# Kernel tuning notes

Measured on AMD Instinct MI355X. Metric: run time of the kernel, lower is better.

Reference implementation:

```python
import jax, jax.numpy as jnp
import numpy as np

B, N, M = 8, 4096, 4096


def setup_inputs() -> dict:
    key = jax.random.key(0)
    ks = jax.random.split(key, 8)
    return {
        "x_aligned": jax.random.normal(ks[0], (B, N, 3), dtype=jnp.float32),
        "y": jax.random.normal(ks[1], (B, M, 3), dtype=jnp.float32),
        "R": jax.random.normal(ks[2], (B, 3, 3), dtype=jnp.float32),
        "S": jax.random.normal(ks[3], (B, 3), dtype=jnp.float32),
        "t": jax.random.normal(ks[4], (B, 3, 1), dtype=jnp.float32),
        "R_gt": jax.random.normal(ks[5], (B, 3, 3), dtype=jnp.float32),
        "S_gt": jax.random.normal(ks[6], (B, 3), dtype=jnp.float32),
        "t_gt": jax.random.normal(ks[7], (B, 3), dtype=jnp.float32),
    }


def chamfer_distance(x, y):
    # x: [B,N,3], y: [B,M,3]; bidirectional mean squared NN distance
    xn = jnp.sum(x * x, axis=-1)                      # [B,N]
    yn = jnp.sum(y * y, axis=-1)                      # [B,M]
    xy = jnp.einsum('bnd,bmd->bnm', x, y)             # [B,N,M]
    d2 = xn[:, :, None] + yn[:, None, :] - 2.0 * xy   # [B,N,M] squared dists
    cham_x = jnp.mean(jnp.min(d2, axis=2), axis=1)    # [B] x -> y
    cham_y = jnp.mean(jnp.min(d2, axis=1), axis=1)    # [B] y -> x
    return jnp.mean(cham_x) + jnp.mean(cham_y)        # batch mean, summed dirs


def reference(x_aligned, y, R, S, t, R_gt, S_gt, t_gt):
    t = jnp.squeeze(t)                                # [B,3]
    eye = jnp.eye(3, dtype=R.dtype)
    R_loss = jnp.einsum('bij,bkj->bik', R, R_gt) - eye  # R @ R_gt^T - I
    L_reg = (jnp.sum(R_loss * R_loss)
             + jnp.sum((S - S_gt) ** 2)
             + jnp.sum((t - t_gt) ** 2))
    L_chamfer = chamfer_distance(x_aligned, y)
    return L_reg + L_chamfer
```

## Files before the change

### kernel.cpp

```cpp
#include <hip/hip_runtime.h>

#define BB 8
#define NN 4096
#define MC 256
#define NCHUNK (NN / MC)
#define KPT 8
#define TPB 256
#define PTS_PER_BLOCK (TPB * KPT)
#define NPTS (2 * BB * NN)


__global__ __launch_bounds__(TPB) void chamfer_partial(
    const float* __restrict__ X, const float* __restrict__ Y,
    float* __restrict__ partial) {
  __shared__ float4 ly[MC];
  const int tid = threadIdx.x;
  const int zb  = blockIdx.z;
  const int b   = zb & (BB - 1);
  const int dir = zb >> 3;
  const float* pts  = dir ? (Y + b * NN * 3) : (X + b * NN * 3);
  const float* refs = dir ? (X + b * NN * 3) : (Y + b * NN * 3);
  const int c = blockIdx.y;

  {
    const int j = c * MC + tid;
    const float a0 = refs[j * 3 + 0];
    const float a1 = refs[j * 3 + 1];
    const float a2 = refs[j * 3 + 2];
    ly[tid] = make_float4(-2.0f * a0, -2.0f * a1, -2.0f * a2,
                          a0 * a0 + a1 * a1 + a2 * a2);
  }
  __syncthreads();

  float px[KPT], py[KPT], pz[KPT], m[KPT];
  const int p0 = blockIdx.x * PTS_PER_BLOCK + tid;
#pragma unroll
  for (int k = 0; k < KPT; k++) {
    const int p = p0 + k * TPB;
    px[k] = pts[p * 3 + 0];
    py[k] = pts[p * 3 + 1];
    pz[k] = pts[p * 3 + 2];
    m[k] = 1e30f;
  }

#pragma unroll 2
  for (int j = 0; j < MC; j += 2) {
    const float4 w0 = ly[j];
    const float4 w1 = ly[j + 1];
#pragma unroll
    for (int k = 0; k < KPT; k++) {
      const float s0 = fmaf(px[k], w0.x, fmaf(py[k], w0.y, fmaf(pz[k], w0.z, w0.w)));
      const float s1 = fmaf(px[k], w1.x, fmaf(py[k], w1.y, fmaf(pz[k], w1.z, w1.w)));
      m[k] = fminf(m[k], fminf(s0, s1));
    }
  }

#pragma unroll
  for (int k = 0; k < KPT; k++) {
    const int p = p0 + k * TPB;
    const float pn = px[k] * px[k] + py[k] * py[k] + pz[k] * pz[k];
    partial[(c * (2 * BB) + zb) * NN + p] = m[k] + pn;
  }
}

__global__ __launch_bounds__(256) void chamfer_reduce(
    const float* __restrict__ partial,
    const float* __restrict__ R, const float* __restrict__ S,
    const float* __restrict__ t, const float* __restrict__ Rgt,
    const float* __restrict__ Sgt, const float* __restrict__ tgt,
    float* __restrict__ out) {
  const int tid = threadIdx.x;
  const int q0 = blockIdx.x * 1024 + tid;
  float s = 0.0f;
#pragma unroll
  for (int kk = 0; kk < 4; kk++) {
    const int q = q0 + kk * 256;
    float m = 1e30f;
#pragma unroll
    for (int c = 0; c < NCHUNK; c++)
      m = fminf(m, partial[c * NPTS + q]);
    s += m;
  }
  for (int o = 32; o > 0; o >>= 1) s += __shfl_down(s, o);
  __shared__ float wsum[4];
  if ((tid & 63) == 0) wsum[tid >> 6] = s;
  __syncthreads();
  if (tid == 0) {
    const float bs = wsum[0] + wsum[1] + wsum[2] + wsum[3];
    atomicAdd(out, bs * (1.0f / (float)(BB * NN)));
  }

  if (blockIdx.x == 0) {
    float v = 0.0f;
    if (tid < 72) {
      const int b = tid / 9, ik = tid % 9, i = ik / 3, k = ik % 3;
      const float* Rb = R + b * 9;
      const float* Gb = Rgt + b * 9;
      float d = Rb[i * 3 + 0] * Gb[k * 3 + 0] +
                Rb[i * 3 + 1] * Gb[k * 3 + 1] +
                Rb[i * 3 + 2] * Gb[k * 3 + 2];
      d -= (i == k) ? 1.0f : 0.0f;
      v = d * d;
    } else if (tid < 96) {
      const int i = tid - 72;
      const float d = S[i] - Sgt[i];
      v = d * d;
    } else if (tid < 120) {
      const int i = tid - 96;
      const float d = t[i] - tgt[i];
      v = d * d;
    }
    for (int o = 32; o > 0; o >>= 1) v += __shfl_down(v, o);
    __shared__ float rsum[4];
    if ((tid & 63) == 0) rsum[tid >> 6] = v;
    __syncthreads();
    if (tid == 0) atomicAdd(out, rsum[0] + rsum[1] + rsum[2] + rsum[3]);
  }
}

extern "C" void kernel_launch(void* const* d_in, const int* in_sizes, int n_in,
                              void* d_out, int out_size, void* d_ws, size_t ws_size,
                              hipStream_t stream) {
  const float* X   = (const float*)d_in[0];
  const float* Y   = (const float*)d_in[1];
  const float* R   = (const float*)d_in[2];
  const float* S   = (const float*)d_in[3];
  const float* t   = (const float*)d_in[4];
  const float* Rgt = (const float*)d_in[5];
  const float* Sgt = (const float*)d_in[6];
  const float* tgt = (const float*)d_in[7];

  float* partial = (float*)d_ws;
  float* out     = (float*)d_out;

  hipMemsetAsync(out, 0, sizeof(float), stream);

  dim3 gA(NN / PTS_PER_BLOCK, NCHUNK, 2 * BB);
  chamfer_partial<<<gA, TPB, 0, stream>>>(X, Y, partial);

  chamfer_reduce<<<NPTS / 1024, 256, 0, stream>>>(partial, R, S, t, Rgt, Sgt, tgt, out);
}
```

Before: 94.56 us.

## Halve points per thread, prefetch LDS refs, fold memset into kernel

Reduces points per thread from 8 to 4, doubling the block count of the distance kernel for better occupancy across CUs. The inner loop now processes four reference points per step and prefetches the next four from LDS. The separate memset of the output is replaced by zeroing it inside the first kernel, and the reduce kernel uses more blocks with one point per thread. The trade-off is lower register reuse per LDS read and more atomics in the reduction.

Measured after the change: 91.46 us. 1.03x faster.

```diff
diff --git a/kernel.cpp b/kernel.cpp
--- a/kernel.cpp
+++ b/kernel.cpp
@@ -4,7 +4,7 @@
 #define NN 4096
 #define MC 256
 #define NCHUNK (NN / MC)
-#define KPT 8
+#define KPT 4
 #define TPB 256
 #define PTS_PER_BLOCK (TPB * KPT)
 #define NPTS (2 * BB * NN)
@@ -12,7 +12,7 @@
 
 __global__ __launch_bounds__(TPB) void chamfer_partial(
     const float* __restrict__ X, const float* __restrict__ Y,
-    float* __restrict__ partial) {
+    float* __restrict__ partial, float* __restrict__ out) {
   __shared__ float4 ly[MC];
   const int tid = threadIdx.x;
   const int zb  = blockIdx.z;
@@ -21,6 +21,9 @@
   const float* pts  = dir ? (Y + b * NN * 3) : (X + b * NN * 3);
   const float* refs = dir ? (X + b * NN * 3) : (Y + b * NN * 3);
   const int c = blockIdx.y;
+
+  if (tid == 0 && blockIdx.x == 0 && blockIdx.y == 0 && blockIdx.z == 0)
+    *out = 0.0f;
 
   {
     const int j = c * MC + tid;
@@ -43,17 +46,31 @@
     m[k] = 1e30f;
   }
 
+#define CHAMFER_BODY(w0, w1, w2, w3)                                           \
+  _Pragma("unroll") for (int k = 0; k < KPT; k++) {                            \
+    const float s0 =                                                           \
+        fmaf(px[k], w0.x, fmaf(py[k], w0.y, fmaf(pz[k], w0.z, w0.w)));         \
+    const float s1 =                                                           \
+        fmaf(px[k], w1.x, fmaf(py[k], w1.y, fmaf(pz[k], w1.z, w1.w)));         \
+    const float s2 =                                                           \
+        fmaf(px[k], w2.x, fmaf(py[k], w2.y, fmaf(pz[k], w2.z, w2.w)));         \
+    const float s3 =                                                           \
+        fmaf(px[k], w3.x, fmaf(py[k], w3.y, fmaf(pz[k], w3.z, w3.w)));         \
+    m[k] = fminf(m[k], fminf(fminf(s0, s1), fminf(s2, s3)));                   \
+  }
+
+  float4 w0 = ly[0], w1 = ly[1], w2 = ly[2], w3 = ly[3];
 #pragma unroll 2
-  for (int j = 0; j < MC; j += 2) {
-    const float4 w0 = ly[j];
-    const float4 w1 = ly[j + 1];
-#pragma unroll
-    for (int k = 0; k < KPT; k++) {
-      const float s0 = fmaf(px[k], w0.x, fmaf(py[k], w0.y, fmaf(pz[k], w0.z, w0.w)));
-      const float s1 = fmaf(px[k], w1.x, fmaf(py[k], w1.y, fmaf(pz[k], w1.z, w1.w)));
-      m[k] = fminf(m[k], fminf(s0, s1));
-    }
+  for (int j = 0; j < MC - 4; j += 4) {
+    const float4 n0 = ly[j + 4];
+    const float4 n1 = ly[j + 5];
+    const float4 n2 = ly[j + 6];
+    const float4 n3 = ly[j + 7];
+    CHAMFER_BODY(w0, w1, w2, w3)
+    w0 = n0; w1 = n1; w2 = n2; w3 = n3;
   }
+  CHAMFER_BODY(w0, w1, w2, w3)
+#undef CHAMFER_BODY
 
 #pragma unroll
   for (int k = 0; k < KPT; k++) {
@@ -70,17 +87,12 @@
     const float* __restrict__ Sgt, const float* __restrict__ tgt,
     float* __restrict__ out) {
   const int tid = threadIdx.x;
-  const int q0 = blockIdx.x * 1024 + tid;
-  float s = 0.0f;
+  const int q = blockIdx.x * 256 + tid;
+  float m = 1e30f;
 #pragma unroll
-  for (int kk = 0; kk < 4; kk++) {
-    const int q = q0 + kk * 256;
-    float m = 1e30f;
-#pragma unroll
-    for (int c = 0; c < NCHUNK; c++)
-      m = fminf(m, partial[c * NPTS + q]);
-    s += m;
-  }
+  for (int c = 0; c < NCHUNK; c++)
+    m = fminf(m, partial[c * NPTS + q]);
+  float s = m;
   for (int o = 32; o > 0; o >>= 1) s += __shfl_down(s, o);
   __shared__ float wsum[4];
   if ((tid & 63) == 0) wsum[tid >> 6] = s;
@@ -133,10 +145,8 @@
   float* partial = (float*)d_ws;
   float* out     = (float*)d_out;
 
-  hipMemsetAsync(out, 0, sizeof(float), stream);
+  dim3 gA(NN / PTS_PER_BLOCK, NCHUNK, 2 * BB);
+  chamfer_partial<<<gA, TPB, 0, stream>>>(X, Y, partial, out);
 
-  dim3 gA(NN / PTS_PER_BLOCK, NCHUNK, 2 * BB);
-  chamfer_partial<<<gA, TPB, 0, stream>>>(X, Y, partial);
-
-  chamfer_reduce<<<NPTS / 1024, 256, 0, stream>>>(partial, R, S, t, Rgt, Sgt, tgt, out);
+  chamfer_reduce<<<NPTS / 256, 256, 0, stream>>>(partial, R, S, t, Rgt, Sgt, tgt, out);
 }
```
